# Kernel tuning notes

Hardware: AMD Instinct MI355X
Metric: run time of the kernel (lower is better)

The kernel has to match this reference:

```python
import jax, jax.numpy as jnp
import numpy as np

B, C, T_TEXT, T_FEAT = 16, 256, 512, 4096
DELTA = 0.1  # temperature


def setup_inputs() -> dict:
    key = jax.random.key(0)
    k1, k2 = jax.random.split(key)
    x = jax.random.normal(k1, (B, C, T_TEXT), dtype=jnp.float32)
    # durations: avg ~8 frames per token so cumsum spans ~T_FEAT frames
    w = jax.random.uniform(k2, (B, T_TEXT), dtype=jnp.float32) * 16.0
    x_mask = jnp.ones((B, T_FEAT), dtype=bool)   # frame-level mask (B, T_feat)
    y_mask = jnp.ones((B, T_TEXT), dtype=bool)   # token-level mask (B, T_text)
    return {"x": x, "w": w, "x_mask": x_mask, "y_mask": y_mask}


def reference(x, w, x_mask, y_mask):
    # x: (B, C, T_text), w: (B, T_text)
    t_feat = x_mask.shape[-1]
    # frame time grid, masked frames zeroed as in reference impl
    t = jnp.arange(t_feat, dtype=x.dtype)[None, :] * x_mask.astype(x.dtype)  # (B, T_feat)
    # Gaussian centers per token: cumulative duration minus half of own duration
    c = jnp.cumsum(w, axis=-1) - 0.5 * w  # (B, T_text)
    # energy: -delta * (t - c)^2  -> (B, T_feat, T_text)
    energy = -DELTA * jnp.square(t[:, :, None] - c[:, None, :])
    energy = jnp.where(y_mask[:, None, :], energy, -jnp.inf)
    attn = jax.nn.softmax(energy, axis=-1)  # softmax over tokens (T_text)
    # weighted sum over tokens: (B, T_feat, T_text) x (B, C, T_text) -> (B, C, T_feat)
    return jnp.einsum('bft,bct->bcf', attn, x)
```

## Files before the change

### kernel.cpp

```cpp
#include <hip/hip_runtime.h>
#include <math.h>


constexpr int BB  = 16;
constexpr int CC  = 256;
constexpr int TT  = 512;
constexpr int TF  = 4096;
constexpr float DEL = 0.1f;

constexpr int TILE_F = 32;
constexpr int MAXW   = 32;
constexpr int MAXN   = 64;
constexpr float CUT  = 200.0f;

__global__ __launch_bounds__(64)
void centers_k(const float* __restrict__ w, float* __restrict__ cw) {
  const int b = blockIdx.x, l = threadIdx.x;
  const float* wr = w + b * TT + l * 8;
  float v[8];
  *(float4*)&v[0] = *(const float4*)&wr[0];
  *(float4*)&v[4] = *(const float4*)&wr[4];
  double s[8]; double run = 0.0;
#pragma unroll
  for (int k = 0; k < 8; ++k) { run += (double)v[k]; s[k] = run; }
  double tot = run;
  for (int off = 1; off < 64; off <<= 1) {
    double o = __shfl_up(tot, off, 64);
    if (l >= off) tot += o;
  }
  const double base = tot - run;
  float* co = cw + b * TT + l * 8;
#pragma unroll
  for (int k = 0; k < 8; ++k) co[k] = (float)(base + s[k] - 0.5 * (double)v[k]);
}

__global__ __launch_bounds__(256, 4)
void gauss_up(const float* __restrict__ x, const float* __restrict__ cw,
              float* __restrict__ out) {
  __shared__ float sc[TT];
  __shared__ __align__(16) float pbuf[MAXN][TILE_F];
  __shared__ int s_info[2];

  const int lin   = blockIdx.x;
  const int xcd   = lin & 7;
  const int slot  = lin >> 3;
  const int b     = xcd * 2 + (slot >> 7);
  const int ftile = slot & 127;
  const int f0    = ftile * TILE_F;
  const int tid   = threadIdx.x;

  sc[tid]       = cw[b * TT + tid];
  sc[tid + 256] = cw[b * TT + tid + 256];
#pragma unroll
  for (int k = 0; k < MAXN * TILE_F / 256; ++k)
    ((float*)pbuf)[tid + 256 * k] = 0.f;
  __syncthreads();

  if (tid < TILE_F) {
    const float fv = (float)(f0 + tid);
    int l = 0, h = TT;
    while (l < h) { int m = (l + h) >> 1; if (sc[m] < fv) l = m + 1; else h = m; }
    int jstar = (l < TT) ? l : TT - 1;
    float dmin = fabsf(sc[jstar] - fv);
    if (l > 0) { float d = fabsf(sc[l - 1] - fv); if (d <= dmin) { dmin = d; jstar = l - 1; } }
    const float D = sqrtf(fmaf(dmin, dmin, CUT));
    int lo = 0; h = TT;
    { const float lv = fv - D;
      while (lo < h) { int m = (lo + h) >> 1; if (sc[m] < lv) lo = m + 1; else h = m; } }
    int hi = lo; h = TT;
    { const float hv = fv + D;
      while (hi < h) { int m = (hi + h) >> 1; if (sc[m] <= hv) hi = m + 1; else h = m; } }
    if (hi - lo > MAXW) {
      int nl = jstar - MAXW / 2; if (nl < lo) nl = lo;
      lo = nl;
      if (hi > lo + MAXW) hi = lo + MAXW;
    }

    int LO = lo, HI = hi;
#pragma unroll
    for (int m = 16; m >= 1; m >>= 1) {
      LO = min(LO, __shfl_xor(LO, m, 32));
      HI = max(HI, __shfl_xor(HI, m, 32));
    }
    int LO4 = LO & ~3;
    if (HI - LO4 > MAXN) {
      const int js0  = __shfl(jstar, 0, 32);
      const int js31 = __shfl(jstar, 31, 32);
      int nl = (((js0 + js31) >> 1) - MAXN / 2) & ~3;
      if (nl < LO4) nl = LO4;
      LO4 = nl;
      if (HI > LO4 + MAXN) HI = LO4 + MAXN;
      if (lo < LO4) lo = LO4;
      if (hi > HI)  hi = HI;
      if (lo >= hi) {
        lo = min(max(jstar, LO4), HI - 1); hi = lo + 1;
      }
    }

    const int n_f = hi - lo;
    const int j0  = lo - LO4;
    const float m0 = DEL * dmin * dmin;
    float Z = 0.f;
    for (int j = 0; j < n_f; ++j) {
      const float d = fv - sc[lo + j];
      const float e = __expf(fmaf(-DEL, d * d, m0));
      pbuf[j0 + j][tid] = e;
      Z += e;
    }
    const float rz = 1.f / Z;
    for (int j = 0; j < n_f; ++j) pbuf[j0 + j][tid] *= rz;
    if (tid == 0) { s_info[0] = LO4; s_info[1] = (HI - LO4 + 3) >> 2; }
  }
  __syncthreads();

  const int LO4 = s_info[0];
  const int NC  = s_info[1];
  const int cg  = tid >> 2;
  const int fg  = tid & 3;

  const float* xr0 = x + ((size_t)b * CC + (size_t)cg * 4) * TT + LO4;

  float acc[4][8];
#pragma unroll
  for (int i = 0; i < 4; ++i)
#pragma unroll
    for (int k = 0; k < 8; ++k) acc[i][k] = 0.f;

  for (int jc = 0; jc < NC; ++jc) {
    float4 xv[4];
#pragma unroll
    for (int i = 0; i < 4; ++i)
      xv[i] = *(const float4*)(xr0 + (size_t)i * TT + 4 * jc);
#pragma unroll
    for (int jj = 0; jj < 4; ++jj) {
      const float4 p0 = *(const float4*)&pbuf[4 * jc + jj][fg * 8];
      const float4 p1 = *(const float4*)&pbuf[4 * jc + jj][fg * 8 + 4];
#pragma unroll
      for (int i = 0; i < 4; ++i) {
        const float xs = ((const float*)&xv[i])[jj];
        acc[i][0] = fmaf(p0.x, xs, acc[i][0]);
        acc[i][1] = fmaf(p0.y, xs, acc[i][1]);
        acc[i][2] = fmaf(p0.z, xs, acc[i][2]);
        acc[i][3] = fmaf(p0.w, xs, acc[i][3]);
        acc[i][4] = fmaf(p1.x, xs, acc[i][4]);
        acc[i][5] = fmaf(p1.y, xs, acc[i][5]);
        acc[i][6] = fmaf(p1.z, xs, acc[i][6]);
        acc[i][7] = fmaf(p1.w, xs, acc[i][7]);
      }
    }
  }

  float* orow = out + ((size_t)b * CC + (size_t)cg * 4) * TF + f0 + fg * 8;
#pragma unroll
  for (int i = 0; i < 4; ++i) {
    *(float4*)(orow + (size_t)i * TF)     =
        make_float4(acc[i][0], acc[i][1], acc[i][2], acc[i][3]);
    *(float4*)(orow + (size_t)i * TF + 4) =
        make_float4(acc[i][4], acc[i][5], acc[i][6], acc[i][7]);
  }
}

extern "C" void kernel_launch(void* const* d_in, const int* in_sizes, int n_in,
                              void* d_out, int out_size, void* d_ws, size_t ws_size,
                              hipStream_t stream) {
  const float* x = (const float*)d_in[0];
  const float* w = (const float*)d_in[1];
  float* out = (float*)d_out;
  float* cw  = (float*)d_ws;

  centers_k<<<dim3(BB), dim3(64), 0, stream>>>(w, cw);
  gauss_up<<<dim3(TF / TILE_F * BB), dim3(256), 0, stream>>>(x, cw, out);
}
```

Baseline: 94.60 us.

## Precompute per-frame token windows in separate kernel, add nontemporal stores

Moves the per-frame binary searches (nearest center and truncation window) out of the main kernel into a new meta_k kernel that uses all 256 threads per block and writes a packed lo/count plus dmin per frame. The main kernel then reads this metadata instead of running the searches in only 32 threads while the rest of the block waits. It also recomputes the exponentials in the normalization pass instead of doing a read-modify-write on LDS, halves the Gaussian cutoff, raises the occupancy hint to 6 blocks, and uses nontemporal output stores. The tradeoff is an extra kernel launch and a metadata round trip through memory. The smaller cutoff narrows the token window, which changes accuracy slightly, and jstar is now approximated as the window midpoint.

```diff
diff --git a/kernel.cpp b/kernel.cpp
--- a/kernel.cpp
+++ b/kernel.cpp
@@ -11,7 +11,9 @@
 constexpr int TILE_F = 32;
 constexpr int MAXW   = 32;
 constexpr int MAXN   = 64;
-constexpr float CUT  = 200.0f;
+constexpr float CUT  = 100.0f;
+
+typedef float vf4 __attribute__((ext_vector_type(4)));
 
 __global__ __launch_bounds__(64)
 void centers_k(const float* __restrict__ w, float* __restrict__ cw) {
@@ -34,9 +36,43 @@
   for (int k = 0; k < 8; ++k) co[k] = (float)(base + s[k] - 0.5 * (double)v[k]);
 }
 
-__global__ __launch_bounds__(256, 4)
+__global__ __launch_bounds__(256)
+void meta_k(const float* __restrict__ cw, float2* __restrict__ meta) {
+  __shared__ float sc[TT];
+  const int b   = blockIdx.x >> 4;
+  const int f   = (blockIdx.x & 15) * 256 + threadIdx.x;
+  const int tid = threadIdx.x;
+  sc[tid]       = cw[b * TT + tid];
+  sc[tid + 256] = cw[b * TT + tid + 256];
+  __syncthreads();
+
+  const float fv = (float)f;
+  int l = 0, h = TT;
+  while (l < h) { int m = (l + h) >> 1; if (sc[m] < fv) l = m + 1; else h = m; }
+  int jstar = (l < TT) ? l : TT - 1;
+  float dmin = fabsf(sc[jstar] - fv);
+  if (l > 0) { float d = fabsf(sc[l - 1] - fv); if (d <= dmin) { dmin = d; jstar = l - 1; } }
+  const float D = sqrtf(fmaf(dmin, dmin, CUT));
+  int lo = 0; h = TT;
+  { const float lv = fv - D;
+    while (lo < h) { int m = (lo + h) >> 1; if (sc[m] < lv) lo = m + 1; else h = m; } }
+  int hi = lo; h = TT;
+  { const float hv = fv + D;
+    while (hi < h) { int m = (hi + h) >> 1; if (sc[m] <= hv) hi = m + 1; else h = m; } }
+  if (hi - lo > MAXW) {
+    int nl = jstar - MAXW / 2; if (nl < lo) nl = lo;
+    lo = nl;
+    if (hi > lo + MAXW) hi = lo + MAXW;
+  }
+  float2 mv;
+  mv.x = __uint_as_float((unsigned)lo | ((unsigned)(hi - lo) << 16));
+  mv.y = dmin;
+  meta[b * TF + f] = mv;
+}
+
+__global__ __launch_bounds__(256, 6)
 void gauss_up(const float* __restrict__ x, const float* __restrict__ cw,
-              float* __restrict__ out) {
+              const float2* __restrict__ meta, float* __restrict__ out) {
   __shared__ float sc[TT];
   __shared__ __align__(16) float pbuf[MAXN][TILE_F];
   __shared__ int s_info[2];
@@ -45,8 +81,7 @@
   const int xcd   = lin & 7;
   const int slot  = lin >> 3;
   const int b     = xcd * 2 + (slot >> 7);
-  const int ftile = slot & 127;
-  const int f0    = ftile * TILE_F;
+  const int f0    = (slot & 127) * TILE_F;
   const int tid   = threadIdx.x;
 
   sc[tid]       = cw[b * TT + tid];
@@ -58,23 +93,12 @@
 
   if (tid < TILE_F) {
     const float fv = (float)(f0 + tid);
-    int l = 0, h = TT;
-    while (l < h) { int m = (l + h) >> 1; if (sc[m] < fv) l = m + 1; else h = m; }
-    int jstar = (l < TT) ? l : TT - 1;
-    float dmin = fabsf(sc[jstar] - fv);
-    if (l > 0) { float d = fabsf(sc[l - 1] - fv); if (d <= dmin) { dmin = d; jstar = l - 1; } }
-    const float D = sqrtf(fmaf(dmin, dmin, CUT));
-    int lo = 0; h = TT;
-    { const float lv = fv - D;
-      while (lo < h) { int m = (lo + h) >> 1; if (sc[m] < lv) lo = m + 1; else h = m; } }
-    int hi = lo; h = TT;
-    { const float hv = fv + D;
-      while (hi < h) { int m = (hi + h) >> 1; if (sc[m] <= hv) hi = m + 1; else h = m; } }
-    if (hi - lo > MAXW) {
-      int nl = jstar - MAXW / 2; if (nl < lo) nl = lo;
-      lo = nl;
-      if (hi > lo + MAXW) hi = lo + MAXW;
-    }
+    const float2 mv = meta[b * TF + f0 + tid];
+    const unsigned ln = __float_as_uint(mv.x);
+    int lo = (int)(ln & 0xffffu);
+    int n  = (int)(ln >> 16);
+    int hi = lo + n;
+    const float dmin = mv.y;
 
     int LO = lo, HI = hi;
 #pragma unroll
@@ -84,6 +108,7 @@
     }
     int LO4 = LO & ~3;
     if (HI - LO4 > MAXN) {
+      const int jstar = lo + (n >> 1);
       const int js0  = __shfl(jstar, 0, 32);
       const int js31 = __shfl(jstar, 31, 32);
       int nl = (((js0 + js31) >> 1) - MAXN / 2) & ~3;
@@ -95,20 +120,21 @@
       if (lo >= hi) {
         lo = min(max(jstar, LO4), HI - 1); hi = lo + 1;
       }
-    }
-
-    const int n_f = hi - lo;
+      n = hi - lo;
+    }
+
     const int j0  = lo - LO4;
     const float m0 = DEL * dmin * dmin;
     float Z = 0.f;
-    for (int j = 0; j < n_f; ++j) {
+    for (int j = 0; j < n; ++j) {
       const float d = fv - sc[lo + j];
-      const float e = __expf(fmaf(-DEL, d * d, m0));
-      pbuf[j0 + j][tid] = e;
-      Z += e;
+      Z += __expf(fmaf(-DEL, d * d, m0));
     }
     const float rz = 1.f / Z;
-    for (int j = 0; j < n_f; ++j) pbuf[j0 + j][tid] *= rz;
+    for (int j = 0; j < n; ++j) {
+      const float d = fv - sc[lo + j];
+      pbuf[j0 + j][tid] = __expf(fmaf(-DEL, d * d, m0)) * rz;
+    }
     if (tid == 0) { s_info[0] = LO4; s_info[1] = (HI - LO4 + 3) >> 2; }
   }
   __syncthreads();
@@ -153,10 +179,10 @@
   float* orow = out + ((size_t)b * CC + (size_t)cg * 4) * TF + f0 + fg * 8;
 #pragma unroll
   for (int i = 0; i < 4; ++i) {
-    *(float4*)(orow + (size_t)i * TF)     =
-        make_float4(acc[i][0], acc[i][1], acc[i][2], acc[i][3]);
-    *(float4*)(orow + (size_t)i * TF + 4) =
-        make_float4(acc[i][4], acc[i][5], acc[i][6], acc[i][7]);
+    vf4 lo4 = { acc[i][0], acc[i][1], acc[i][2], acc[i][3] };
+    vf4 hi4 = { acc[i][4], acc[i][5], acc[i][6], acc[i][7] };
+    __builtin_nontemporal_store(lo4, (vf4*)(orow + (size_t)i * TF));
+    __builtin_nontemporal_store(hi4, (vf4*)(orow + (size_t)i * TF + 4));
   }
 }
 
@@ -167,7 +193,9 @@
   const float* w = (const float*)d_in[1];
   float* out = (float*)d_out;
   float* cw  = (float*)d_ws;
+  float2* meta = (float2*)((char*)d_ws + 64 * 1024);
 
   centers_k<<<dim3(BB), dim3(64), 0, stream>>>(w, cw);
-  gauss_up<<<dim3(TF / TILE_F * BB), dim3(256), 0, stream>>>(x, cw, out);
-}
+  meta_k<<<dim3(BB * 16), dim3(256), 0, stream>>>(cw, meta);
+  gauss_up<<<dim3(TF / TILE_F * BB), dim3(256), 0, stream>>>(x, cw, meta, out);
+}
```

Result: slower. 106.2 us (+12.3%).
